# Kernel optimization log

Measured on AMD Instinct MI355X. Metric: run time of the kernel, lower is better.

## Reference

```python
import jax, jax.numpy as jnp
import numpy as np

# Standard TCN TemporalBlock (Bai et al.): dilated causal conv -> chomp -> relu ->
# (dropout, identity at eval) x2, plus 1x1-conv residual, final relu.
# PyTorch pads (k-1)*d on both sides then chomps the right, which equals
# left-only causal padding of (k-1)*d.

def _causal_conv(x, w, b, dilation):
    pad = (w.shape[-1] - 1) * dilation
    y = jax.lax.conv_general_dilated(
        x, w, window_strides=(1,), padding=[(pad, 0)],
        rhs_dilation=(dilation,), dimension_numbers=('NCH', 'OIH', 'NCH'))
    return y + b[None, :, None]

def _block(x, w1, b1, w2, b2, wd, bd, dil):
    h = jax.nn.relu(_causal_conv(x, w1, b1, dil))
    h = jax.nn.relu(_causal_conv(h, w2, b2, dil))
    res = _causal_conv(x, wd, bd, 1)  # 1x1 downsample (channel counts differ)
    return jax.nn.relu(h + res)

def setup_inputs() -> dict:
    key = jax.random.key(0)
    ks = jax.random.split(key, 18)
    B, Cin, L, C1, C2, H, K, O = 4096, 30, 256, 100, 200, 8, 5, 1
    def rn(k, shape, s=0.05):
        return jax.random.normal(k, shape, dtype=jnp.float32) * s
    return {
        'x': rn(ks[0], (B, Cin, L), 1.0),
        'task_labels': jax.random.randint(ks[1], (B,), 0, H),
        # TCN level 0: in_features -> 100, dilation 1
        'w1_0': rn(ks[2], (C1, Cin, K)), 'b1_0': rn(ks[3], (C1,)),
        'w2_0': rn(ks[4], (C1, C1, K)),  'b2_0': rn(ks[5], (C1,)),
        'wd_0': rn(ks[6], (C1, Cin, 1)), 'bd_0': rn(ks[7], (C1,)),
        # TCN level 1: 100 -> 200, dilation 2
        'w1_1': rn(ks[8], (C2, C1, K)),  'b1_1': rn(ks[9], (C2,)),
        'w2_1': rn(ks[10], (C2, C2, K)), 'b2_1': rn(ks[11], (C2,)),
        'wd_1': rn(ks[12], (C2, C1, 1)), 'bd_1': rn(ks[13], (C2,)),
        # 8 per-task heads, stacked: Linear(200->100), Tanh, Linear(100->1)
        'hw1': rn(ks[14], (H, C1, C2)), 'hb1': rn(ks[15], (H, C1)),
        'hw2': rn(ks[16], (H, O, C1)),  'hb2': rn(ks[17], (H, O)),
    }

def reference(x, task_labels, w1_0, b1_0, w2_0, b2_0, wd_0, bd_0,
              w1_1, b1_1, w2_1, b2_1, wd_1, bd_1, hw1, hb1, hw2, hb2):
    # TCN backbone (eval mode: dropout is identity)
    y = _block(x, w1_0, b1_0, w2_0, b2_0, wd_0, bd_0, 1)
    y = _block(y, w1_1, b1_1, w2_1, b2_1, wd_1, bd_1, 2)
    feat = y[:, :, -1]  # [B, 200] last timestep
    # Vectorized per-task head dispatch: gather each sample's head weights.
    # Mathematically identical to the per-task gather/MLP/scatter loop.
    W1 = hw1[task_labels]  # [B, 100, 200]
    B1 = hb1[task_labels]  # [B, 100]
    W2 = hw2[task_labels]  # [B, 1, 100]
    B2 = hb2[task_labels]  # [B, 1]
    h = jnp.tanh(jnp.einsum('bd,bod->bo', feat, W1) + B1)
    return jnp.einsum('bo,bpo->bp', h, W2) + B2  # [B, 1]
```

## Files before the change

kernel.cpp:

```cpp
#include <hip/hip_runtime.h>
#include <math.h>


#define R     4096
#define CIN   30
#define LSEQ  256
#define C1    100
#define C2    200
#define KW    5
#define T0    231
#define WIN   25
#define NU0   21
#define NJ0   9
#define NT1   5

#define ROW_XT    0
#define ROW_H0T   750
#define ROW_Y0T   2850
#define ROW_H1T   0
#define ROW_FEAT  3750

__global__ __launch_bounds__(1024) void k_tr(const float* __restrict__ x,
                                             float* __restrict__ xT) {
  const int l = threadIdx.x & 63;
  const int wv = threadIdx.x >> 6;
  const int b = blockIdx.x * 64 + l;
  const float* xb = x + (size_t)b * (CIN * LSEQ) + T0;
  for (int r = wv; r < CIN * WIN; r += 16) {
    const int ci = r / WIN;
    const int u = r - ci * WIN;
    xT[(size_t)r * R + b] = xb[ci * LSEQ + u];
  }
}

__global__ __launch_bounds__(256) void k1(const float* __restrict__ xT,
                                          const float* __restrict__ w1,
                                          const float* __restrict__ b1,
                                          float* __restrict__ h0T) {
  __shared__ float wT[CIN * KW * 16];
  const int tid = threadIdx.x;
  const int ctile = blockIdx.y * 16;
  for (int idx = tid; idx < CIN * KW * 16; idx += 256) {
    const int kk = idx >> 4, cl = idx & 15, c = ctile + cl;
    wT[idx] = (c < C1) ? w1[c * (CIN * KW) + kk] : 0.f;
  }
  __syncthreads();
  const int l = tid & 63, wv = tid >> 6;
  const int b = blockIdx.x * 64 + l;
  const int cb = ctile + wv * 4;
  float acc[4][NU0];
#pragma unroll
  for (int m = 0; m < 4; ++m) {
    const float bias = (cb + m < C1) ? b1[cb + m] : 0.f;
#pragma unroll
    for (int u = 0; u < NU0; ++u) acc[m][u] = bias;
  }
  for (int ci = 0; ci < CIN; ++ci) {
    float xr[WIN];
    const float* xp = xT + (size_t)ci * WIN * R + b;
#pragma unroll
    for (int u = 0; u < WIN; ++u) xr[u] = xp[(size_t)u * R];
#pragma unroll
    for (int k = 0; k < KW; ++k) {
      const float4 w = *reinterpret_cast<const float4*>(&wT[(ci * KW + k) * 16 + wv * 4]);
#pragma unroll
      for (int u = 0; u < NU0; ++u) {
        acc[0][u] = fmaf(xr[u + k], w.x, acc[0][u]);
        acc[1][u] = fmaf(xr[u + k], w.y, acc[1][u]);
        acc[2][u] = fmaf(xr[u + k], w.z, acc[2][u]);
        acc[3][u] = fmaf(xr[u + k], w.w, acc[3][u]);
      }
    }
  }
#pragma unroll
  for (int m = 0; m < 4; ++m) {
    const int c = cb + m;
    if (c < C1) {
#pragma unroll
      for (int u = 0; u < NU0; ++u)
        h0T[(size_t)(c * NU0 + u) * R + b] = fmaxf(acc[m][u], 0.f);
    }
  }
}

__global__ __launch_bounds__(256) void k2(const float* __restrict__ xT,
                                          const float* __restrict__ h0T,
                                          const float* __restrict__ w2,
                                          const float* __restrict__ b2,
                                          const float* __restrict__ wd,
                                          const float* __restrict__ bd,
                                          float* __restrict__ y0T) {
  __shared__ float wT[C1 * KW * 16];
  __shared__ float wdT[CIN * 16];
  const int tid = threadIdx.x;
  const int ctile = blockIdx.y * 16;
  for (int idx = tid; idx < C1 * KW * 16; idx += 256) {
    const int kk = idx >> 4, cl = idx & 15, c = ctile + cl;
    wT[idx] = (c < C1) ? w2[c * (C1 * KW) + kk] : 0.f;
  }
  for (int idx = tid; idx < CIN * 16; idx += 256) {
    const int ci = idx >> 4, cl = idx & 15, c = ctile + cl;
    wdT[idx] = (c < C1) ? wd[c * CIN + ci] : 0.f;
  }
  __syncthreads();
  const int l = tid & 63, wv = tid >> 6;
  const int b = blockIdx.x * 64 + l;
  const int cb = ctile + wv * 4;
  float acc[4][NJ0], rac[4][NJ0];
#pragma unroll
  for (int m = 0; m < 4; ++m) {
    const float bias = (cb + m < C1) ? b2[cb + m] : 0.f;
    const float bres = (cb + m < C1) ? bd[cb + m] : 0.f;
#pragma unroll
    for (int j = 0; j < NJ0; ++j) { acc[m][j] = bias; rac[m][j] = bres; }
  }
  for (int ci = 0; ci < C1; ++ci) {
    float hr[NU0];
    const float* hp = h0T + (size_t)ci * NU0 * R + b;
#pragma unroll
    for (int u = 0; u < NU0; ++u) hr[u] = hp[(size_t)u * R];
#pragma unroll
    for (int k = 0; k < KW; ++k) {
      const float4 w = *reinterpret_cast<const float4*>(&wT[(ci * KW + k) * 16 + wv * 4]);
#pragma unroll
      for (int j = 0; j < NJ0; ++j) {
        acc[0][j] = fmaf(hr[2 * j + k], w.x, acc[0][j]);
        acc[1][j] = fmaf(hr[2 * j + k], w.y, acc[1][j]);
        acc[2][j] = fmaf(hr[2 * j + k], w.z, acc[2][j]);
        acc[3][j] = fmaf(hr[2 * j + k], w.w, acc[3][j]);
      }
    }
  }
  for (int ci = 0; ci < CIN; ++ci) {
    float xr[NJ0];
    const float* xp = xT + (size_t)(ci * WIN + 8) * R + b;
#pragma unroll
    for (int j = 0; j < NJ0; ++j) xr[j] = xp[(size_t)(2 * j) * R];
    const float4 w = *reinterpret_cast<const float4*>(&wdT[ci * 16 + wv * 4]);
#pragma unroll
    for (int j = 0; j < NJ0; ++j) {
      rac[0][j] = fmaf(xr[j], w.x, rac[0][j]);
      rac[1][j] = fmaf(xr[j], w.y, rac[1][j]);
      rac[2][j] = fmaf(xr[j], w.z, rac[2][j]);
      rac[3][j] = fmaf(xr[j], w.w, rac[3][j]);
    }
  }
#pragma unroll
  for (int m = 0; m < 4; ++m) {
    const int c = cb + m;
    if (c < C1) {
#pragma unroll
      for (int j = 0; j < NJ0; ++j)
        y0T[(size_t)(c * NJ0 + j) * R + b] =
            fmaxf(fmaxf(acc[m][j], 0.f) + rac[m][j], 0.f);
    }
  }
}

__global__ __launch_bounds__(256) void k3(const float* __restrict__ y0T,
                                          const float* __restrict__ w1,
                                          const float* __restrict__ b1,
                                          float* __restrict__ h1T) {
  __shared__ float wT[C1 * KW * 16];
  const int tid = threadIdx.x;
  const int ctile = blockIdx.y * 16;
  for (int idx = tid; idx < C1 * KW * 16; idx += 256) {
    const int kk = idx >> 4, cl = idx & 15, c = ctile + cl;
    wT[idx] = (c < C2) ? w1[c * (C1 * KW) + kk] : 0.f;
  }
  __syncthreads();
  const int l = tid & 63, wv = tid >> 6;
  const int b = blockIdx.x * 64 + l;
  const int cb = ctile + wv * 4;
  float acc[4][NT1];
#pragma unroll
  for (int m = 0; m < 4; ++m) {
    const float bias = (cb + m < C2) ? b1[cb + m] : 0.f;
#pragma unroll
    for (int t = 0; t < NT1; ++t) acc[m][t] = bias;
  }
  for (int ci = 0; ci < C1; ++ci) {
    float yr[NJ0];
    const float* yp = y0T + (size_t)ci * NJ0 * R + b;
#pragma unroll
    for (int u = 0; u < NJ0; ++u) yr[u] = yp[(size_t)u * R];
#pragma unroll
    for (int k = 0; k < KW; ++k) {
      const float4 w = *reinterpret_cast<const float4*>(&wT[(ci * KW + k) * 16 + wv * 4]);
#pragma unroll
      for (int t = 0; t < NT1; ++t) {
        acc[0][t] = fmaf(yr[t + k], w.x, acc[0][t]);
        acc[1][t] = fmaf(yr[t + k], w.y, acc[1][t]);
        acc[2][t] = fmaf(yr[t + k], w.z, acc[2][t]);
        acc[3][t] = fmaf(yr[t + k], w.w, acc[3][t]);
      }
    }
  }
#pragma unroll
  for (int m = 0; m < 4; ++m) {
    const int c = cb + m;
    if (c < C2) {
#pragma unroll
      for (int t = 0; t < NT1; ++t)
        h1T[(size_t)(c * NT1 + t) * R + b] = fmaxf(acc[m][t], 0.f);
    }
  }
}

__global__ __launch_bounds__(256) void k4a(const float* __restrict__ h1T,
                                           const float* __restrict__ y0T,
                                           const float* __restrict__ w2,
                                           const float* __restrict__ b2,
                                           const float* __restrict__ wd,
                                           const float* __restrict__ bd,
                                           float* __restrict__ featT) {
  __shared__ float wT[C2 * KW * 8];
  __shared__ float wdT[C1 * 8];
  const int tid = threadIdx.x;
  const int cb8 = blockIdx.y * 8;
  for (int idx = tid; idx < C2 * KW * 8; idx += 256) {
    const int kk = idx >> 3, cl = idx & 7;
    wT[idx] = w2[(cb8 + cl) * (C2 * KW) + kk];
  }
  for (int idx = tid; idx < C1 * 8; idx += 256) {
    const int ci = idx >> 3, cl = idx & 7;
    wdT[idx] = wd[(cb8 + cl) * C1 + ci];
  }
  __syncthreads();
  const int l = tid & 63, wv = tid >> 6;
  const int b4 = blockIdx.x * 256 + l * 4;
  const int c0 = cb8 + wv * 2;
  float a0[4], a1[4], r0[4], r1[4];
  {
    const float bA = b2[c0], bB = b2[c0 + 1];
    const float dA = bd[c0], dB = bd[c0 + 1];
#pragma unroll
    for (int m = 0; m < 4; ++m) { a0[m] = bA; a1[m] = bB; r0[m] = dA; r1[m] = dB; }
  }
#pragma unroll 4
  for (int kk = 0; kk < C2 * KW; ++kk) {
    const float4 h = *reinterpret_cast<const float4*>(&h1T[(size_t)kk * R + b4]);
    const float2 w = *reinterpret_cast<const float2*>(&wT[kk * 8 + wv * 2]);
    a0[0] = fmaf(h.x, w.x, a0[0]); a0[1] = fmaf(h.y, w.x, a0[1]);
    a0[2] = fmaf(h.z, w.x, a0[2]); a0[3] = fmaf(h.w, w.x, a0[3]);
    a1[0] = fmaf(h.x, w.y, a1[0]); a1[1] = fmaf(h.y, w.y, a1[1]);
    a1[2] = fmaf(h.z, w.y, a1[2]); a1[3] = fmaf(h.w, w.y, a1[3]);
  }
#pragma unroll 4
  for (int ci = 0; ci < C1; ++ci) {
    const float4 y = *reinterpret_cast<const float4*>(&y0T[(size_t)(ci * NJ0 + 8) * R + b4]);
    const float2 w = *reinterpret_cast<const float2*>(&wdT[ci * 8 + wv * 2]);
    r0[0] = fmaf(y.x, w.x, r0[0]); r0[1] = fmaf(y.y, w.x, r0[1]);
    r0[2] = fmaf(y.z, w.x, r0[2]); r0[3] = fmaf(y.w, w.x, r0[3]);
    r1[0] = fmaf(y.x, w.y, r1[0]); r1[1] = fmaf(y.y, w.y, r1[1]);
    r1[2] = fmaf(y.z, w.y, r1[2]); r1[3] = fmaf(y.w, w.y, r1[3]);
  }
  float4 f0, f1;
  f0.x = fmaxf(fmaxf(a0[0], 0.f) + r0[0], 0.f);
  f0.y = fmaxf(fmaxf(a0[1], 0.f) + r0[1], 0.f);
  f0.z = fmaxf(fmaxf(a0[2], 0.f) + r0[2], 0.f);
  f0.w = fmaxf(fmaxf(a0[3], 0.f) + r0[3], 0.f);
  f1.x = fmaxf(fmaxf(a1[0], 0.f) + r1[0], 0.f);
  f1.y = fmaxf(fmaxf(a1[1], 0.f) + r1[1], 0.f);
  f1.z = fmaxf(fmaxf(a1[2], 0.f) + r1[2], 0.f);
  f1.w = fmaxf(fmaxf(a1[3], 0.f) + r1[3], 0.f);
  *reinterpret_cast<float4*>(&featT[(size_t)c0 * R + b4]) = f0;
  *reinterpret_cast<float4*>(&featT[(size_t)(c0 + 1) * R + b4]) = f1;
}

__global__ __launch_bounds__(256) void k4b(const float* __restrict__ featT,
                                           const int* __restrict__ labels,
                                           const float* __restrict__ hw1,
                                           const float* __restrict__ hb1,
                                           const float* __restrict__ hw2,
                                           const float* __restrict__ hb2,
                                           float* __restrict__ out) {
  __shared__ float fs[4][C2];
  const int tid = threadIdx.x;
  const int b0 = blockIdx.x * 4;
  for (int idx = tid; idx < 4 * C2; idx += 256) {
    const int c = idx >> 2, bi = idx & 3;
    fs[bi][c] = featT[(size_t)c * R + b0 + bi];
  }
  __syncthreads();
  const int l = tid & 63, wv = tid >> 6;
  const int b = b0 + wv;
  const int task = labels[b];
  const float* W1 = hw1 + (size_t)task * (C1 * C2);
  const float* fp = fs[wv];
  float p = 0.f;
  {
    float a = hb1[task * C1 + l];
    const float* wr = W1 + (size_t)l * C2;
#pragma unroll 4
    for (int d = 0; d < C2; d += 4) {
      const float4 fv = *reinterpret_cast<const float4*>(&fp[d]);
      const float4 wv4 = *reinterpret_cast<const float4*>(&wr[d]);
      a = fmaf(fv.x, wv4.x, a); a = fmaf(fv.y, wv4.y, a);
      a = fmaf(fv.z, wv4.z, a); a = fmaf(fv.w, wv4.w, a);
    }
    p = tanhf(a) * hw2[task * C1 + l];
  }
  if (l < C1 - 64) {
    const int o = 64 + l;
    float a = hb1[task * C1 + o];
    const float* wr = W1 + (size_t)o * C2;
#pragma unroll 4
    for (int d = 0; d < C2; d += 4) {
      const float4 fv = *reinterpret_cast<const float4*>(&fp[d]);
      const float4 wv4 = *reinterpret_cast<const float4*>(&wr[d]);
      a = fmaf(fv.x, wv4.x, a); a = fmaf(fv.y, wv4.y, a);
      a = fmaf(fv.z, wv4.z, a); a = fmaf(fv.w, wv4.w, a);
    }
    p = fmaf(tanhf(a), hw2[task * C1 + o], p);
  }
#pragma unroll
  for (int off = 32; off > 0; off >>= 1) p += __shfl_down(p, off, 64);
  if (l == 0) out[b] = p + hb2[task];
}

extern "C" void kernel_launch(void* const* d_in, const int* in_sizes, int n_in,
                              void* d_out, int out_size, void* d_ws, size_t ws_size,
                              hipStream_t stream) {
  const float* x    = (const float*)d_in[0];
  const int* labels = (const int*)d_in[1];
  const float* w1_0 = (const float*)d_in[2];
  const float* b1_0 = (const float*)d_in[3];
  const float* w2_0 = (const float*)d_in[4];
  const float* b2_0 = (const float*)d_in[5];
  const float* wd_0 = (const float*)d_in[6];
  const float* bd_0 = (const float*)d_in[7];
  const float* w1_1 = (const float*)d_in[8];
  const float* b1_1 = (const float*)d_in[9];
  const float* w2_1 = (const float*)d_in[10];
  const float* b2_1 = (const float*)d_in[11];
  const float* wd_1 = (const float*)d_in[12];
  const float* bd_1 = (const float*)d_in[13];
  const float* hw1  = (const float*)d_in[14];
  const float* hb1  = (const float*)d_in[15];
  const float* hw2  = (const float*)d_in[16];
  const float* hb2  = (const float*)d_in[17];
  float* out = (float*)d_out;

  float* ws    = (float*)d_ws;
  float* xT    = ws + (size_t)ROW_XT * R;
  float* h0T   = ws + (size_t)ROW_H0T * R;
  float* y0T   = ws + (size_t)ROW_Y0T * R;
  float* h1T   = ws + (size_t)ROW_H1T * R;
  float* featT = ws + (size_t)ROW_FEAT * R;

  hipLaunchKernelGGL(k_tr, dim3(64), dim3(1024), 0, stream, x, xT);
  hipLaunchKernelGGL(k1, dim3(64, 7), dim3(256), 0, stream, xT, w1_0, b1_0, h0T);
  hipLaunchKernelGGL(k2, dim3(64, 7), dim3(256), 0, stream, xT, h0T, w2_0, b2_0, wd_0, bd_0, y0T);
  hipLaunchKernelGGL(k3, dim3(64, 13), dim3(256), 0, stream, y0T, w1_1, b1_1, h1T);
  hipLaunchKernelGGL(k4a, dim3(16, 25), dim3(256), 0, stream, h1T, y0T, w2_1, b2_1, wd_1, bd_1, featT);
  hipLaunchKernelGGL(k4b, dim3(1024), dim3(256), 0, stream, featT, labels,
                     hw1, hb1, hw2, hb2, out);
}
```

Before: 596.3 us.

## Stage activations in shared memory, retile k4a, transpose head weights for coalescing

Each conv kernel now stages chunks of its transposed activation input in LDS instead of reading the same global rows from every channel-tile wave. Weight staging into LDS is rewritten so global reads are contiguous. k4a is retiled to 64 batch by 32 channels with LDS-staged activations and weights. k_tr gets a 2D grid with smaller blocks, and a new kernel transposes the head weights so k4b reads them coalesced across lanes. The cost is more syncthreads and LDS use, which may lower occupancy, plus an extra weight-transpose launch on every call.

Result: slower. 655.6 us (+9.9%).

```diff
diff --git a/kernel.cpp b/kernel.cpp
--- a/kernel.cpp
+++ b/kernel.cpp
@@ -19,32 +19,45 @@
 #define ROW_Y0T   2850
 #define ROW_H1T   0
 #define ROW_FEAT  3750
-
-__global__ __launch_bounds__(1024) void k_tr(const float* __restrict__ x,
-                                             float* __restrict__ xT) {
-  const int l = threadIdx.x & 63;
-  const int wv = threadIdx.x >> 6;
+#define ROW_HW1T  3950
+
+__global__ __launch_bounds__(256) void k_tr(const float* __restrict__ x,
+                                            float* __restrict__ xT) {
+  const int l = threadIdx.x & 63, wv = threadIdx.x >> 6;
   const int b = blockIdx.x * 64 + l;
   const float* xb = x + (size_t)b * (CIN * LSEQ) + T0;
-  for (int r = wv; r < CIN * WIN; r += 16) {
-    const int ci = r / WIN;
-    const int u = r - ci * WIN;
+  for (int r2 = wv; r2 < 150; r2 += 4) {
+    const int r = blockIdx.y * 150 + r2;
+    const int ci = r / WIN, u = r - ci * WIN;
     xT[(size_t)r * R + b] = xb[ci * LSEQ + u];
   }
 }
 
+__global__ __launch_bounds__(256) void k_trW(const float* __restrict__ hw1,
+                                             float* __restrict__ hw1T) {
+  const int idx = blockIdx.x * 256 + threadIdx.x;
+  if (idx < 8 * C1 * C2) {
+    const int h = idx / (C1 * C2);
+    const int r = idx - h * (C1 * C2);
+    const int o = r / C2, d = r - o * C2;
+    hw1T[h * (C1 * C2) + d * C1 + o] = hw1[idx];
+  }
+}
+
+#define CH1 10
 __global__ __launch_bounds__(256) void k1(const float* __restrict__ xT,
                                           const float* __restrict__ w1,
                                           const float* __restrict__ b1,
                                           float* __restrict__ h0T) {
   __shared__ float wT[CIN * KW * 16];
+  __shared__ float xs[CH1 * WIN * 64];
   const int tid = threadIdx.x;
   const int ctile = blockIdx.y * 16;
   for (int idx = tid; idx < CIN * KW * 16; idx += 256) {
-    const int kk = idx >> 4, cl = idx & 15, c = ctile + cl;
-    wT[idx] = (c < C1) ? w1[c * (CIN * KW) + kk] : 0.f;
-  }
-  __syncthreads();
+    const int cl = idx / (CIN * KW), kk = idx - cl * (CIN * KW);
+    const int c = ctile + cl;
+    wT[kk * 16 + cl] = (c < C1) ? w1[c * (CIN * KW) + kk] : 0.f;
+  }
   const int l = tid & 63, wv = tid >> 6;
   const int b = blockIdx.x * 64 + l;
   const int cb = ctile + wv * 4;
@@ -55,20 +68,28 @@
 #pragma unroll
     for (int u = 0; u < NU0; ++u) acc[m][u] = bias;
   }
-  for (int ci = 0; ci < CIN; ++ci) {
-    float xr[WIN];
-    const float* xp = xT + (size_t)ci * WIN * R + b;
-#pragma unroll
-    for (int u = 0; u < WIN; ++u) xr[u] = xp[(size_t)u * R];
-#pragma unroll
-    for (int k = 0; k < KW; ++k) {
-      const float4 w = *reinterpret_cast<const float4*>(&wT[(ci * KW + k) * 16 + wv * 4]);
-#pragma unroll
-      for (int u = 0; u < NU0; ++u) {
-        acc[0][u] = fmaf(xr[u + k], w.x, acc[0][u]);
-        acc[1][u] = fmaf(xr[u + k], w.y, acc[1][u]);
-        acc[2][u] = fmaf(xr[u + k], w.z, acc[2][u]);
-        acc[3][u] = fmaf(xr[u + k], w.w, acc[3][u]);
+  for (int ch = 0; ch < 3; ++ch) {
+    __syncthreads();
+    for (int idx = tid; idx < CH1 * WIN * 64; idx += 256) {
+      const int rr = idx >> 6, bb = idx & 63;
+      xs[idx] = xT[(size_t)(ch * (CH1 * WIN) + rr) * R + blockIdx.x * 64 + bb];
+    }
+    __syncthreads();
+    for (int cil = 0; cil < CH1; ++cil) {
+      const int ci = ch * CH1 + cil;
+      float xr[WIN];
+#pragma unroll
+      for (int u = 0; u < WIN; ++u) xr[u] = xs[(cil * WIN + u) * 64 + l];
+#pragma unroll
+      for (int k = 0; k < KW; ++k) {
+        const float4 w = *reinterpret_cast<const float4*>(&wT[(ci * KW + k) * 16 + wv * 4]);
+#pragma unroll
+        for (int u = 0; u < NU0; ++u) {
+          acc[0][u] = fmaf(xr[u + k], w.x, acc[0][u]);
+          acc[1][u] = fmaf(xr[u + k], w.y, acc[1][u]);
+          acc[2][u] = fmaf(xr[u + k], w.z, acc[2][u]);
+          acc[3][u] = fmaf(xr[u + k], w.w, acc[3][u]);
+        }
       }
     }
   }
@@ -83,6 +104,7 @@
   }
 }
 
+#define CH2 8
 __global__ __launch_bounds__(256) void k2(const float* __restrict__ xT,
                                           const float* __restrict__ h0T,
                                           const float* __restrict__ w2,
@@ -92,17 +114,19 @@
                                           float* __restrict__ y0T) {
   __shared__ float wT[C1 * KW * 16];
   __shared__ float wdT[CIN * 16];
+  __shared__ float hs[CH2 * NU0 * 64];
   const int tid = threadIdx.x;
   const int ctile = blockIdx.y * 16;
   for (int idx = tid; idx < C1 * KW * 16; idx += 256) {
-    const int kk = idx >> 4, cl = idx & 15, c = ctile + cl;
-    wT[idx] = (c < C1) ? w2[c * (C1 * KW) + kk] : 0.f;
+    const int cl = idx / (C1 * KW), kk = idx - cl * (C1 * KW);
+    const int c = ctile + cl;
+    wT[kk * 16 + cl] = (c < C1) ? w2[c * (C1 * KW) + kk] : 0.f;
   }
   for (int idx = tid; idx < CIN * 16; idx += 256) {
-    const int ci = idx >> 4, cl = idx & 15, c = ctile + cl;
-    wdT[idx] = (c < C1) ? wd[c * CIN + ci] : 0.f;
-  }
-  __syncthreads();
+    const int cl = idx / CIN, ci = idx - cl * CIN;
+    const int c = ctile + cl;
+    wdT[ci * 16 + cl] = (c < C1) ? wd[c * CIN + ci] : 0.f;
+  }
   const int l = tid & 63, wv = tid >> 6;
   const int b = blockIdx.x * 64 + l;
   const int cb = ctile + wv * 4;
@@ -114,23 +138,7 @@
 #pragma unroll
     for (int j = 0; j < NJ0; ++j) { acc[m][j] = bias; rac[m][j] = bres; }
   }
-  for (int ci = 0; ci < C1; ++ci) {
-    float hr[NU0];
-    const float* hp = h0T + (size_t)ci * NU0 * R + b;
-#pragma unroll
-    for (int u = 0; u < NU0; ++u) hr[u] = hp[(size_t)u * R];
-#pragma unroll
-    for (int k = 0; k < KW; ++k) {
-      const float4 w = *reinterpret_cast<const float4*>(&wT[(ci * KW + k) * 16 + wv * 4]);
-#pragma unroll
-      for (int j = 0; j < NJ0; ++j) {
-        acc[0][j] = fmaf(hr[2 * j + k], w.x, acc[0][j]);
-        acc[1][j] = fmaf(hr[2 * j + k], w.y, acc[1][j]);
-        acc[2][j] = fmaf(hr[2 * j + k], w.z, acc[2][j]);
-        acc[3][j] = fmaf(hr[2 * j + k], w.w, acc[3][j]);
-      }
-    }
-  }
+  __syncthreads();
   for (int ci = 0; ci < CIN; ++ci) {
     float xr[NJ0];
     const float* xp = xT + (size_t)(ci * WIN + 8) * R + b;
@@ -145,6 +153,32 @@
       rac[3][j] = fmaf(xr[j], w.w, rac[3][j]);
     }
   }
+  for (int c8 = 0; c8 < 13; ++c8) {
+    const int nci = min(CH2, C1 - c8 * CH2);
+    __syncthreads();
+    for (int idx = tid; idx < nci * NU0 * 64; idx += 256) {
+      const int rr = idx >> 6, bb = idx & 63;
+      hs[idx] = h0T[(size_t)(c8 * CH2 * NU0 + rr) * R + blockIdx.x * 64 + bb];
+    }
+    __syncthreads();
+    for (int cil = 0; cil < nci; ++cil) {
+      const int ci = c8 * CH2 + cil;
+      float hr[NU0];
+#pragma unroll
+      for (int u = 0; u < NU0; ++u) hr[u] = hs[(cil * NU0 + u) * 64 + l];
+#pragma unroll
+      for (int k = 0; k < KW; ++k) {
+        const float4 w = *reinterpret_cast<const float4*>(&wT[(ci * KW + k) * 16 + wv * 4]);
+#pragma unroll
+        for (int j = 0; j < NJ0; ++j) {
+          acc[0][j] = fmaf(hr[2 * j + k], w.x, acc[0][j]);
+          acc[1][j] = fmaf(hr[2 * j + k], w.y, acc[1][j]);
+          acc[2][j] = fmaf(hr[2 * j + k], w.z, acc[2][j]);
+          acc[3][j] = fmaf(hr[2 * j + k], w.w, acc[3][j]);
+        }
+      }
+    }
+  }
 #pragma unroll
   for (int m = 0; m < 4; ++m) {
     const int c = cb + m;
@@ -157,18 +191,20 @@
   }
 }
 
+#define CH3 16
 __global__ __launch_bounds__(256) void k3(const float* __restrict__ y0T,
                                           const float* __restrict__ w1,
                                           const float* __restrict__ b1,
                                           float* __restrict__ h1T) {
   __shared__ float wT[C1 * KW * 16];
+  __shared__ float ys[CH3 * NJ0 * 64];
   const int tid = threadIdx.x;
   const int ctile = blockIdx.y * 16;
   for (int idx = tid; idx < C1 * KW * 16; idx += 256) {
-    const int kk = idx >> 4, cl = idx & 15, c = ctile + cl;
-    wT[idx] = (c < C2) ? w1[c * (C1 * KW) + kk] : 0.f;
-  }
-  __syncthreads();
+    const int cl = idx / (C1 * KW), kk = idx - cl * (C1 * KW);
+    const int c = ctile + cl;
+    wT[kk * 16 + cl] = (c < C2) ? w1[c * (C1 * KW) + kk] : 0.f;
+  }
   const int l = tid & 63, wv = tid >> 6;
   const int b = blockIdx.x * 64 + l;
   const int cb = ctile + wv * 4;
@@ -179,20 +215,29 @@
 #pragma unroll
     for (int t = 0; t < NT1; ++t) acc[m][t] = bias;
   }
-  for (int ci = 0; ci < C1; ++ci) {
-    float yr[NJ0];
-    const float* yp = y0T + (size_t)ci * NJ0 * R + b;
-#pragma unroll
-    for (int u = 0; u < NJ0; ++u) yr[u] = yp[(size_t)u * R];
-#pragma unroll
-    for (int k = 0; k < KW; ++k) {
-      const float4 w = *reinterpret_cast<const float4*>(&wT[(ci * KW + k) * 16 + wv * 4]);
-#pragma unroll
-      for (int t = 0; t < NT1; ++t) {
-        acc[0][t] = fmaf(yr[t + k], w.x, acc[0][t]);
-        acc[1][t] = fmaf(yr[t + k], w.y, acc[1][t]);
-        acc[2][t] = fmaf(yr[t + k], w.z, acc[2][t]);
-        acc[3][t] = fmaf(yr[t + k], w.w, acc[3][t]);
+  for (int c16 = 0; c16 < 7; ++c16) {
+    const int nci = min(CH3, C1 - c16 * CH3);
+    __syncthreads();
+    for (int idx = tid; idx < nci * NJ0 * 64; idx += 256) {
+      const int rr = idx >> 6, bb = idx & 63;
+      ys[idx] = y0T[(size_t)(c16 * CH3 * NJ0 + rr) * R + blockIdx.x * 64 + bb];
+    }
+    __syncthreads();
+    for (int cil = 0; cil < nci; ++cil) {
+      const int ci = c16 * CH3 + cil;
+      float yr[NJ0];
+#pragma unroll
+      for (int u = 0; u < NJ0; ++u) yr[u] = ys[(cil * NJ0 + u) * 64 + l];
+#pragma unroll
+      for (int k = 0; k < KW; ++k) {
+        const float4 w = *reinterpret_cast<const float4*>(&wT[(ci * KW + k) * 16 + wv * 4]);
+#pragma unroll
+        for (int t = 0; t < NT1; ++t) {
+          acc[0][t] = fmaf(yr[t + k], w.x, acc[0][t]);
+          acc[1][t] = fmaf(yr[t + k], w.y, acc[1][t]);
+          acc[2][t] = fmaf(yr[t + k], w.z, acc[2][t]);
+          acc[3][t] = fmaf(yr[t + k], w.w, acc[3][t]);
+        }
       }
     }
   }
@@ -207,6 +252,7 @@
   }
 }
 
+#define KC4 100
 __global__ __launch_bounds__(256) void k4a(const float* __restrict__ h1T,
                                            const float* __restrict__ y0T,
                                            const float* __restrict__ w2,
@@ -214,63 +260,73 @@
                                            const float* __restrict__ wd,
                                            const float* __restrict__ bd,
                                            float* __restrict__ featT) {
-  __shared__ float wT[C2 * KW * 8];
-  __shared__ float wdT[C1 * 8];
+  __shared__ float as[KC4 * 64];
+  __shared__ float wc[KC4 * 32];
   const int tid = threadIdx.x;
-  const int cb8 = blockIdx.y * 8;
-  for (int idx = tid; idx < C2 * KW * 8; idx += 256) {
-    const int kk = idx >> 3, cl = idx & 7;
-    wT[idx] = w2[(cb8 + cl) * (C2 * KW) + kk];
-  }
-  for (int idx = tid; idx < C1 * 8; idx += 256) {
-    const int ci = idx >> 3, cl = idx & 7;
-    wdT[idx] = wd[(cb8 + cl) * C1 + ci];
+  const int ctile = blockIdx.y * 32;
+  const int l = tid & 63, wv = tid >> 6;
+  const int b = blockIdx.x * 64 + l;
+  const int c0 = ctile + wv * 8;
+  float acc[8], rs[8];
+#pragma unroll
+  for (int m = 0; m < 8; ++m) {
+    const int c = c0 + m;
+    acc[m] = (c < C2) ? b2[c] : 0.f;
+    rs[m] = (c < C2) ? bd[c] : 0.f;
+  }
+  for (int ph = 0; ph < 10; ++ph) {
+    __syncthreads();
+    for (int idx = tid; idx < KC4 * 64; idx += 256) {
+      const int rr = idx >> 6, bb = idx & 63;
+      as[idx] = h1T[(size_t)(ph * KC4 + rr) * R + blockIdx.x * 64 + bb];
+    }
+    for (int idx = tid; idx < KC4 * 32; idx += 256) {
+      const int cl = idx / KC4, kk = idx - cl * KC4;
+      const int c = ctile + cl;
+      wc[kk * 32 + cl] = (c < C2) ? w2[(size_t)c * (C2 * KW) + ph * KC4 + kk] : 0.f;
+    }
+    __syncthreads();
+    for (int kkl = 0; kkl < KC4; ++kkl) {
+      const float a = as[kkl * 64 + l];
+      const float4 w0 = *reinterpret_cast<const float4*>(&wc[kkl * 32 + wv * 8]);
+      const float4 w1_ = *reinterpret_cast<const float4*>(&wc[kkl * 32 + wv * 8 + 4]);
+      acc[0] = fmaf(a, w0.x, acc[0]); acc[1] = fmaf(a, w0.y, acc[1]);
+      acc[2] = fmaf(a, w0.z, acc[2]); acc[3] = fmaf(a, w0.w, acc[3]);
+      acc[4] = fmaf(a, w1_.x, acc[4]); acc[5] = fmaf(a, w1_.y, acc[5]);
+      acc[6] = fmaf(a, w1_.z, acc[6]); acc[7] = fmaf(a, w1_.w, acc[7]);
+    }
   }
   __syncthreads();
-  const int l = tid & 63, wv = tid >> 6;
-  const int b4 = blockIdx.x * 256 + l * 4;
-  const int c0 = cb8 + wv * 2;
-  float a0[4], a1[4], r0[4], r1[4];
-  {
-    const float bA = b2[c0], bB = b2[c0 + 1];
-    const float dA = bd[c0], dB = bd[c0 + 1];
-#pragma unroll
-    for (int m = 0; m < 4; ++m) { a0[m] = bA; a1[m] = bB; r0[m] = dA; r1[m] = dB; }
-  }
-#pragma unroll 4
-  for (int kk = 0; kk < C2 * KW; ++kk) {
-    const float4 h = *reinterpret_cast<const float4*>(&h1T[(size_t)kk * R + b4]);
-    const float2 w = *reinterpret_cast<const float2*>(&wT[kk * 8 + wv * 2]);
-    a0[0] = fmaf(h.x, w.x, a0[0]); a0[1] = fmaf(h.y, w.x, a0[1]);
-    a0[2] = fmaf(h.z, w.x, a0[2]); a0[3] = fmaf(h.w, w.x, a0[3]);
-    a1[0] = fmaf(h.x, w.y, a1[0]); a1[1] = fmaf(h.y, w.y, a1[1]);
-    a1[2] = fmaf(h.z, w.y, a1[2]); a1[3] = fmaf(h.w, w.y, a1[3]);
-  }
-#pragma unroll 4
+  for (int idx = tid; idx < C1 * 64; idx += 256) {
+    const int rr = idx >> 6, bb = idx & 63;
+    as[idx] = y0T[(size_t)(rr * NJ0 + 8) * R + blockIdx.x * 64 + bb];
+  }
+  for (int idx = tid; idx < C1 * 32; idx += 256) {
+    const int cl = idx / C1, ci = idx - cl * C1;
+    const int c = ctile + cl;
+    wc[ci * 32 + cl] = (c < C2) ? wd[c * C1 + ci] : 0.f;
+  }
+  __syncthreads();
   for (int ci = 0; ci < C1; ++ci) {
-    const float4 y = *reinterpret_cast<const float4*>(&y0T[(size_t)(ci * NJ0 + 8) * R + b4]);
-    const float2 w = *reinterpret_cast<const float2*>(&wdT[ci * 8 + wv * 2]);
-    r0[0] = fmaf(y.x, w.x, r0[0]); r0[1] = fmaf(y.y, w.x, r0[1]);
-    r0[2] = fmaf(y.z, w.x, r0[2]); r0[3] = fmaf(y.w, w.x, r0[3]);
-    r1[0] = fmaf(y.x, w.y, r1[0]); r1[1] = fmaf(y.y, w.y, r1[1]);
-    r1[2] = fmaf(y.z, w.y, r1[2]); r1[3] = fmaf(y.w, w.y, r1[3]);
-  }
-  float4 f0, f1;
-  f0.x = fmaxf(fmaxf(a0[0], 0.f) + r0[0], 0.f);
-  f0.y = fmaxf(fmaxf(a0[1], 0.f) + r0[1], 0.f);
-  f0.z = fmaxf(fmaxf(a0[2], 0.f) + r0[2], 0.f);
-  f0.w = fmaxf(fmaxf(a0[3], 0.f) + r0[3], 0.f);
-  f1.x = fmaxf(fmaxf(a1[0], 0.f) + r1[0], 0.f);
-  f1.y = fmaxf(fmaxf(a1[1], 0.f) + r1[1], 0.f);
-  f1.z = fmaxf(fmaxf(a1[2], 0.f) + r1[2], 0.f);
-  f1.w = fmaxf(fmaxf(a1[3], 0.f) + r1[3], 0.f);
-  *reinterpret_cast<float4*>(&featT[(size_t)c0 * R + b4]) = f0;
-  *reinterpret_cast<float4*>(&featT[(size_t)(c0 + 1) * R + b4]) = f1;
+    const float a = as[ci * 64 + l];
+    const float4 w0 = *reinterpret_cast<const float4*>(&wc[ci * 32 + wv * 8]);
+    const float4 w1_ = *reinterpret_cast<const float4*>(&wc[ci * 32 + wv * 8 + 4]);
+    rs[0] = fmaf(a, w0.x, rs[0]); rs[1] = fmaf(a, w0.y, rs[1]);
+    rs[2] = fmaf(a, w0.z, rs[2]); rs[3] = fmaf(a, w0.w, rs[3]);
+    rs[4] = fmaf(a, w1_.x, rs[4]); rs[5] = fmaf(a, w1_.y, rs[5]);
+    rs[6] = fmaf(a, w1_.z, rs[6]); rs[7] = fmaf(a, w1_.w, rs[7]);
+  }
+#pragma unroll
+  for (int m = 0; m < 8; ++m) {
+    const int c = c0 + m;
+    if (c < C2)
+      featT[(size_t)c * R + b] = fmaxf(fmaxf(acc[m], 0.f) + rs[m], 0.f);
+  }
 }
 
 __global__ __launch_bounds__(256) void k4b(const float* __restrict__ featT,
                                            const int* __restrict__ labels,
-                                           const float* __restrict__ hw1,
+                                           const float* __restrict__ hw1T,
                                            const float* __restrict__ hb1,
                                            const float* __restrict__ hw2,
                                            const float* __restrict__ hb2,
@@ -286,34 +342,18 @@
   const int l = tid & 63, wv = tid >> 6;
   const int b = b0 + wv;
   const int task = labels[b];
-  const float* W1 = hw1 + (size_t)task * (C1 * C2);
+  const float* Wt = hw1T + (size_t)task * (C1 * C2);
   const float* fp = fs[wv];
-  float p = 0.f;
-  {
-    float a = hb1[task * C1 + l];
-    const float* wr = W1 + (size_t)l * C2;
-#pragma unroll 4
-    for (int d = 0; d < C2; d += 4) {
-      const float4 fv = *reinterpret_cast<const float4*>(&fp[d]);
-      const float4 wv4 = *reinterpret_cast<const float4*>(&wr[d]);
-      a = fmaf(fv.x, wv4.x, a); a = fmaf(fv.y, wv4.y, a);
-      a = fmaf(fv.z, wv4.z, a); a = fmaf(fv.w, wv4.w, a);
-    }
-    p = tanhf(a) * hw2[task * C1 + l];
-  }
-  if (l < C1 - 64) {
-    const int o = 64 + l;
-    float a = hb1[task * C1 + o];
-    const float* wr = W1 + (size_t)o * C2;
-#pragma unroll 4
-    for (int d = 0; d < C2; d += 4) {
-      const float4 fv = *reinterpret_cast<const float4*>(&fp[d]);
-      const float4 wv4 = *reinterpret_cast<const float4*>(&wr[d]);
-      a = fmaf(fv.x, wv4.x, a); a = fmaf(fv.y, wv4.y, a);
-      a = fmaf(fv.z, wv4.z, a); a = fmaf(fv.w, wv4.w, a);
-    }
-    p = fmaf(tanhf(a), hw2[task * C1 + o], p);
-  }
+  float a0 = hb1[task * C1 + l];
+  float a1 = (l < C1 - 64) ? hb1[task * C1 + 64 + l] : 0.f;
+  for (int d = 0; d < C2; ++d) {
+    const float fd = fp[d];
+    const float* row = Wt + d * C1;
+    a0 = fmaf(fd, row[l], a0);
+    if (l < C1 - 64) a1 = fmaf(fd, row[64 + l], a1);
+  }
+  float p = tanhf(a0) * hw2[task * C1 + l];
+  if (l < C1 - 64) p = fmaf(tanhf(a1), hw2[task * C1 + 64 + l], p);
 #pragma unroll
   for (int off = 32; off > 0; off >>= 1) p += __shfl_down(p, off, 64);
   if (l == 0) out[b] = p + hb2[task];
@@ -348,12 +388,14 @@
   float* y0T   = ws + (size_t)ROW_Y0T * R;
   float* h1T   = ws + (size_t)ROW_H1T * R;
   float* featT = ws + (size_t)ROW_FEAT * R;
-
-  hipLaunchKernelGGL(k_tr, dim3(64), dim3(1024), 0, stream, x, xT);
+  float* hw1T  = ws + (size_t)ROW_HW1T * R;
+
+  hipLaunchKernelGGL(k_trW, dim3(625), dim3(256), 0, stream, hw1, hw1T);
+  hipLaunchKernelGGL(k_tr, dim3(64, 5), dim3(256), 0, stream, x, xT);
   hipLaunchKernelGGL(k1, dim3(64, 7), dim3(256), 0, stream, xT, w1_0, b1_0, h0T);
   hipLaunchKernelGGL(k2, dim3(64, 7), dim3(256), 0, stream, xT, h0T, w2_0, b2_0, wd_0, bd_0, y0T);
   hipLaunchKernelGGL(k3, dim3(64, 13), dim3(256), 0, stream, y0T, w1_1, b1_1, h1T);
-  hipLaunchKernelGGL(k4a, dim3(16, 25), dim3(256), 0, stream, h1T, y0T, w2_1, b2_1, wd_1, bd_1, featT);
+  hipLaunchKernelGGL(k4a, dim3(64, 7), dim3(256), 0, stream, h1T, y0T, w2_1, b2_1, wd_1, bd_1, featT);
   hipLaunchKernelGGL(k4b, dim3(1024), dim3(256), 0, stream, featT, labels,
-                     hw1, hb1, hw2, hb2, out);
-}
+                     hw1T, hb1, hw2, hb2, out);
+}
```
